# Kernel optimization log

Measured on AMD Instinct MI355X. Metric: run time of the kernel, lower is better.

Reference implementation:

```python
import jax, jax.numpy as jnp
import numpy as np

N, E, G = 50000, 800000, 1024      # nodes, edges, graphs
NF, R, H, O, B = 32, 4, 64, 16, 2  # node vocab, relations, hidden, output, conv blocks
MAX_DEG = 10                       # PyG MFConv default max_degree


def setup_inputs() -> dict:
    key = jax.random.key(0)
    ks = jax.random.split(key, 32)
    s = 0.05
    inp = {
        "x": jax.random.normal(ks[0], (N, NF), jnp.float32),
        "edge_attr": jax.random.normal(ks[1], (E, R), jnp.float32),
        "edge_index": jax.random.randint(ks[2], (2, E), 0, N),
        "batch_idx": jnp.sort(jax.random.randint(ks[3], (N,), 0, G)),
        "emb": jax.random.normal(ks[4], (NF, H), jnp.float32) * s,
        "lin1_w": jax.random.normal(ks[5], (H, H), jnp.float32) * s,
        "lin1_b": jnp.zeros((H,), jnp.float32),
        "lin2_w": jax.random.normal(ks[6], (H, O), jnp.float32) * s,
        "lin2_b": jnp.zeros((O,), jnp.float32),
    }
    for b in range(B):
        k = 7 + 4 * b
        inp[f"rgcn_w{b}"] = jax.random.normal(ks[k], (R, H, H), jnp.float32) * s
        inp[f"rgcn_root{b}"] = jax.random.normal(ks[k + 1], (H, H), jnp.float32) * s
        inp[f"rgcn_b{b}"] = jnp.zeros((H,), jnp.float32)
        inp[f"mf_wl{b}"] = jax.random.normal(ks[k + 2], (MAX_DEG + 1, H, H), jnp.float32) * s
        inp[f"mf_bl{b}"] = jnp.zeros((MAX_DEG + 1, H), jnp.float32)
        inp[f"mf_wr{b}"] = jax.random.normal(ks[k + 3], (MAX_DEG + 1, H, H), jnp.float32) * s
    return inp


def _rgcn(h, src, tgt, rel, W, Wroot, bias):
    # PyG RGCNConv: per-relation linear transform + per-(node,relation) MEAN aggregation + root + bias.
    hx = jnp.einsum('nh,rho->rno', h, W)            # [R,N,H] transformed features per relation
    m = hx[rel, src]                                # [E,H] per-edge messages
    seg = tgt * R + rel                             # segment id per (target node, relation)
    cnt = jax.ops.segment_sum(jnp.ones((E,), h.dtype), seg, num_segments=N * R)
    inv = jnp.where(cnt > 0, 1.0 / cnt, 0.0)
    agg = jax.ops.segment_sum(m * inv[seg][:, None], tgt, num_segments=N)
    return agg + h @ Wroot + bias


def _mfconv(h, src, tgt, Wl, bl, Wr):
    # PyG MFConv: sum-aggregate neighbors, then degree-indexed linear layers (lin_l has bias, lin_r none).
    deg = jnp.clip(jax.ops.segment_sum(jnp.ones((E,), jnp.int32), tgt, num_segments=N), 0, MAX_DEG)
    agg = jax.ops.segment_sum(h[src], tgt, num_segments=N)   # [N,H]
    out = jnp.zeros_like(h)
    for d in range(MAX_DEG + 1):                    # fixed small set of degree buckets
        mask = (deg == d)[:, None]
        out = out + jnp.where(mask, agg @ Wl[d] + bl[d] + h @ Wr[d], 0.0)
    return out


def reference(x, edge_index, edge_attr, batch_idx, emb,
              rgcn_w0, rgcn_root0, rgcn_b0, mf_wl0, mf_bl0, mf_wr0,
              rgcn_w1, rgcn_root1, rgcn_b1, mf_wl1, mf_bl1, mf_wr1,
              lin1_w, lin1_b, lin2_w, lin2_b):
    src, tgt = edge_index[0], edge_index[1]
    rel = jnp.argmax(edge_attr, axis=-1)
    h = emb[jnp.argmax(x, axis=-1)]                 # node embedding lookup
    blocks = [(rgcn_w0, rgcn_root0, rgcn_b0, mf_wl0, mf_bl0, mf_wr0),
              (rgcn_w1, rgcn_root1, rgcn_b1, mf_wl1, mf_bl1, mf_wr1)]
    for (W, Wro, bi, Wl, bl, Wr) in blocks:
        h = jax.nn.relu(h)
        h = _rgcn(h, src, tgt, rel, W, Wro, bi)
        h = jax.nn.relu(h)
        h = _mfconv(h, src, tgt, Wl, bl, Wr)
    g = jax.ops.segment_sum(h, batch_idx, num_segments=G)   # global add pool
    g = jax.nn.relu(g @ lin1_w + lin1_b)
    return g @ lin2_w + lin2_b
```

## Files before the change

kernel.cpp:

```cpp
#include <hip/hip_runtime.h>
#include <hip/hip_fp16.h>
#include <cstdint>
#include <cstddef>

#define Nn 50000
#define Ne 800000
#define Ng 1024
#define NFd 32
#define Rr 4
#define Hd 64
#define Od 16
#define MAXD 10
#define NSEG (Nn * Rr)
#define SCAN_BLK ((NSEG + 255) / 256)
#define ORDER_SZ (Nn + 48)
#define NB_MF ((ORDER_SZ + 15) / 16)
#define NB_RG (Nn / 16)
#define NB_RELSEG (Ne / 256)
#define NB_EMBED (Nn / 4)
#define WT_PER_LAYER (Hd * 5 * Hd)

typedef _Float16 f16x8 __attribute__((ext_vector_type(8)));
typedef float f32x4 __attribute__((ext_vector_type(4)));

__device__ __forceinline__ float reluf(float v) { return v > 0.f ? v : 0.f; }
__device__ __forceinline__ int rfl(int v) { return __builtin_amdgcn_readfirstlane(v); }

__global__ void k_rel_emb(const float4* __restrict__ ea, const int* __restrict__ eidx,
                          int* __restrict__ seg, int* __restrict__ rank,
                          int* __restrict__ cnt,
                          const float* __restrict__ x, const float* __restrict__ emb,
                          float* __restrict__ h, __half* __restrict__ h16) {
    if (blockIdx.x < NB_RELSEG) {
        int e = blockIdx.x * 256 + threadIdx.x;
        float4 a = ea[e];
        int bi = 0; float bv = a.x;
        if (a.y > bv) { bv = a.y; bi = 1; }
        if (a.z > bv) { bv = a.z; bi = 2; }
        if (a.w > bv) { bv = a.w; bi = 3; }
        int s = eidx[Ne + e] * Rr + bi;
        seg[e] = s;
        rank[e] = atomicAdd(&cnt[s], 1);
    } else {
        int wave = ((blockIdx.x - NB_RELSEG) * 256 + threadIdx.x) >> 6;
        int lane = threadIdx.x & 63;
        float v = (lane < NFd) ? x[(size_t)wave * NFd + lane] : -1e30f;
        int idx = lane;
        #pragma unroll
        for (int off = 16; off >= 1; off >>= 1) {
            float ov = __shfl_down(v, off);
            int oi = __shfl_down(idx, off);
            if (ov > v || (ov == v && oi < idx)) { v = ov; idx = oi; }
        }
        idx = __shfl(idx, 0);
        float hv = reluf(emb[(size_t)idx * Hd + lane]);
        h[(size_t)wave * Hd + lane] = hv;
        h16[(size_t)wave * Hd + lane] = __float2half(hv);
    }
}

__global__ void k_prep_wt(const float* __restrict__ w0, const float* __restrict__ r0,
                          const float* __restrict__ w1, const float* __restrict__ r1,
                          __half* __restrict__ wt) {
    int idx = blockIdx.x * 256 + threadIdx.x;
    if (idx >= 2 * WT_PER_LAYER) return;
    int b = idx / WT_PER_LAYER;
    int rem = idx % WT_PER_LAYER;
    int c = rem / 320;
    int k = rem % 320;
    const float* W  = b ? w1 : w0;
    const float* Rt = b ? r1 : r0;
    float v = (k < 64) ? Rt[k * Hd + c]
                       : W[((size_t)((k - 64) >> 6)) * Hd * Hd + ((k - 64) & 63) * Hd + c];
    wt[idx] = __float2half(v);
}

__global__ void k_scan1(const int* __restrict__ cnt, int* __restrict__ off,
                        int* __restrict__ bsum, int* __restrict__ bcnt) {
    __shared__ int s[256];
    __shared__ int hist[16];
    int t = threadIdx.x;
    if (t < 16) hist[t] = 0;
    int idx = blockIdx.x * 256 + t;
    int v = (idx < NSEG) ? cnt[idx] : 0;
    s[t] = v;
    __syncthreads();
    if ((t & 3) == 0 && idx < NSEG) {
        int dsum = s[t] + s[t + 1] + s[t + 2] + s[t + 3];
        atomicAdd(&hist[min(dsum, MAXD)], 1);
    }
    #pragma unroll
    for (int o = 1; o < 256; o <<= 1) {
        int x = (t >= o) ? s[t - o] : 0;
        __syncthreads();
        s[t] += x;
        __syncthreads();
    }
    if (idx < NSEG) off[idx] = s[t] - v;
    if (t == 255) bsum[blockIdx.x] = s[255];
    if (t < 16) {
        int h = hist[t];
        if (h > 0) atomicAdd(&bcnt[t], h);
    }
}

__global__ void k_scan2(int* __restrict__ bsum, const int* __restrict__ bcnt,
                        int* __restrict__ bbase, int* __restrict__ order) {
    __shared__ int s[1024];
    int t = threadIdx.x;
    int v = (t < SCAN_BLK) ? bsum[t] : 0;
    s[t] = v;
    __syncthreads();
    #pragma unroll
    for (int o = 1; o < 1024; o <<= 1) {
        int x = (t >= o) ? s[t - o] : 0;
        __syncthreads();
        s[t] += x;
        __syncthreads();
    }
    if (t < SCAN_BLK) bsum[t] = s[t] - v;
    if (t == 0) {
        int run = 0;
        for (int d = 0; d <= MAXD; d++) {
            int c = bcnt[d];
            bbase[d] = run;
            int pad = (c + 3) & ~3;
            for (int i = c; i < pad; i++) order[run + i] = -1;
            run += pad;
        }
        for (int i = run; i < ORDER_SZ; i++) order[i] = -1;
    }
}

__global__ void k_scan3_bucket(int* __restrict__ off, const int* __restrict__ bsum,
                               const int4* __restrict__ cnt4, const int* __restrict__ bbase,
                               int* __restrict__ bfill, int* __restrict__ order) {
    __shared__ int hist[16];
    __shared__ int base[16];
    int t = threadIdx.x;
    if (t < 16) hist[t] = 0;
    __syncthreads();
    int idx = blockIdx.x * 256 + t;
    if (idx == 0) off[NSEG] = Ne;
    if (idx < NSEG) off[idx] = off[idx] + bsum[blockIdx.x];
    int d = 0, rk = 0;
    bool valid = (idx < Nn);
    if (valid) {
        int4 c = cnt4[idx];
        d = min(c.x + c.y + c.z + c.w, MAXD);
        rk = atomicAdd(&hist[d], 1);
    }
    __syncthreads();
    if (t < 16) {
        int h = hist[t];
        base[t] = (h > 0) ? atomicAdd(&bfill[t], h) : 0;
    }
    __syncthreads();
    if (valid) order[bbase[d] + base[d] + rk] = idx | (d << 20);
}

__global__ void k_scatter(const int* __restrict__ eidx, const int* __restrict__ seg,
                          const int* __restrict__ rank, const int* __restrict__ off,
                          int* __restrict__ sorted_src) {
    int e = blockIdx.x * 256 + threadIdx.x;
    if (e >= Ne) return;
    int pos = off[seg[e]] + rank[e];
    sorted_src[pos] = eidx[e];
}

#define H16(ptr, s) __half2float((ptr)[(size_t)(s) * Hd + lane])

__global__ __launch_bounds__(256) void k_rgcn_fused(
        const __half* __restrict__ hin16,
        const int* __restrict__ off, const int* __restrict__ ssrc,
        const __half* __restrict__ wt, const float* __restrict__ bias,
        float* __restrict__ hout, __half* __restrict__ hout16) {
    __shared__ __align__(16) __half alds[16 * 296];
    int tid = threadIdx.x;
    int wv = tid >> 6, lane = tid & 63;
    int nblk = rfl(blockIdx.x * 16);
    int n0 = nblk + wv * 4;
    int ob[17];
    #pragma unroll
    for (int k = 0; k < 17; k++) ob[k] = rfl(off[4 * n0 + k]);

    float acc = 0.f, snap = 0.f;
    int segi = 0;
    int nb = ob[1];
    int e = ob[0], eEnd = ob[16];

#define EMIT_SEG do {                                                \
        float d_ = acc - snap; snap = acc;                           \
        int cN_ = ob[segi + 1] - ob[segi];                           \
        float iv_ = (cN_ > 0) ? 1.f / (float)cN_ : 0.f;              \
        alds[(wv * 4 + (segi >> 2)) * 296 + (segi & 3) * 72 + lane]  \
            = __float2half(d_ * iv_);                                \
        segi++;                                                      \
        nb = (segi < 16) ? ob[segi + 1] : 0x7fffffff;                \
    } while (0)

    if (e + 16 <= eEnd) {
        int4 iA = *(const int4*)(ssrc + e);
        int4 iB = *(const int4*)(ssrc + e + 4);
        int4 iC = *(const int4*)(ssrc + e + 8);
        int4 iD = *(const int4*)(ssrc + e + 12);
        while (true) {
            int en = e + 16;
            bool more = (en + 16 <= eEnd);
            int4 jA, jB, jC, jD;
            if (more) {
                jA = *(const int4*)(ssrc + en);
                jB = *(const int4*)(ssrc + en + 4);
                jC = *(const int4*)(ssrc + en + 8);
                jD = *(const int4*)(ssrc + en + 12);
            }
            float v0 = H16(hin16, iA.x);
            float v1 = H16(hin16, iA.y);
            float v2 = H16(hin16, iA.z);
            float v3 = H16(hin16, iA.w);
            float v4 = H16(hin16, iB.x);
            float v5 = H16(hin16, iB.y);
            float v6 = H16(hin16, iB.z);
            float v7 = H16(hin16, iB.w);
            float v8 = H16(hin16, iC.x);
            float v9 = H16(hin16, iC.y);
            float vA = H16(hin16, iC.z);
            float vB = H16(hin16, iC.w);
            float vC = H16(hin16, iD.x);
            float vD = H16(hin16, iD.y);
            float vE = H16(hin16, iD.z);
            float vF = H16(hin16, iD.w);
            while (e + 0  == nb) EMIT_SEG;  acc += v0;
            while (e + 1  == nb) EMIT_SEG;  acc += v1;
            while (e + 2  == nb) EMIT_SEG;  acc += v2;
            while (e + 3  == nb) EMIT_SEG;  acc += v3;
            while (e + 4  == nb) EMIT_SEG;  acc += v4;
            while (e + 5  == nb) EMIT_SEG;  acc += v5;
            while (e + 6  == nb) EMIT_SEG;  acc += v6;
            while (e + 7  == nb) EMIT_SEG;  acc += v7;
            while (e + 8  == nb) EMIT_SEG;  acc += v8;
            while (e + 9  == nb) EMIT_SEG;  acc += v9;
            while (e + 10 == nb) EMIT_SEG;  acc += vA;
            while (e + 11 == nb) EMIT_SEG;  acc += vB;
            while (e + 12 == nb) EMIT_SEG;  acc += vC;
            while (e + 13 == nb) EMIT_SEG;  acc += vD;
            while (e + 14 == nb) EMIT_SEG;  acc += vE;
            while (e + 15 == nb) EMIT_SEG;  acc += vF;
            e = en;
            if (!more) break;
            iA = jA; iB = jB; iC = jC; iD = jD;
        }
    }
    for (; e < eEnd; e++) {
        while (e == nb) EMIT_SEG;
        int s = rfl(ssrc[e]);
        acc += H16(hin16, s);
    }
    while (segi < 16) EMIT_SEG;
#undef EMIT_SEG

    __syncthreads();

    int rp = lane & 15;
    int g  = lane >> 4;
    const __half* ha = hin16 + (size_t)(nblk + rp) * Hd + 8 * g;
    const __half* ba = wt + (size_t)(wv * 16 + rp) * 320 + 8 * g;
    const __half* aa = alds + rp * 296 + 8 * g;
    f32x4 dacc = {0.f, 0.f, 0.f, 0.f};
    #pragma unroll
    for (int s = 0; s < 10; s++) {
        f16x8 bfrag = *(const f16x8*)(ba + s * 32);
        f16x8 afrag;
        if (s < 2) afrag = *(const f16x8*)(ha + s * 32);
        else       afrag = *(const f16x8*)(aa + ((s - 2) >> 1) * 72 + ((s - 2) & 1) * 32);
        dacc = __builtin_amdgcn_mfma_f32_16x16x32_f16(afrag, bfrag, dacc, 0, 0, 0);
    }
    int c = wv * 16 + rp;
    float bb = bias[c];
    #pragma unroll
    for (int j = 0; j < 4; j++) {
        int row = nblk + g * 4 + j;
        float v = reluf(dacc[j] + bb);
        hout[(size_t)row * Hd + c] = v;
        hout16[(size_t)row * Hd + c] = __float2half(v);
    }
}

__global__ __launch_bounds__(256) void k_mf_fused(
        const float* __restrict__ hin, const __half* __restrict__ hin16,
        const int* __restrict__ off, const int* __restrict__ ssrc,
        const int* __restrict__ order, const float* __restrict__ Wl,
        const float* __restrict__ bl, const float* __restrict__ Wr,
        float* __restrict__ hout, __half* __restrict__ hout16, int relu_out) {
    __shared__ float lds[4][4][Hd];
    int tid = threadIdx.x;
    int wv = tid >> 6, lane = tid & 63;
    int slot0 = rfl(blockIdx.x * 16 + wv * 4);
    int ent[4];
    #pragma unroll
    for (int i = 0; i < 4; i++) ent[i] = rfl(order[slot0 + i]);
    int d = -1;
    #pragma unroll
    for (int i = 3; i >= 0; i--) if (ent[i] >= 0) d = ent[i] >> 20;
    if (d < 0) return;
    int n[4];
    #pragma unroll
    for (int i = 0; i < 4; i++) n[i] = (ent[i] >= 0) ? (ent[i] & 0xFFFFF) : 0;
    for (int i = 0; i < 4; i++) {
        int e0 = rfl(off[n[i] * Rr]);
        int e4 = rfl(off[n[i] * Rr + Rr]);
        float p0 = 0.f, p1 = 0.f, p2 = 0.f, p3 = 0.f;
        int e = e0;
        for (; e + 16 <= e4; e += 16) {
            const int4 sA = *(const int4*)(ssrc + e);
            const int4 sB = *(const int4*)(ssrc + e + 4);
            const int4 sC = *(const int4*)(ssrc + e + 8);
            const int4 sD = *(const int4*)(ssrc + e + 12);
            p0 += H16(hin16, sA.x) + H16(hin16, sA.y) + H16(hin16, sA.z) + H16(hin16, sA.w);
            p1 += H16(hin16, sB.x) + H16(hin16, sB.y) + H16(hin16, sB.z) + H16(hin16, sB.w);
            p2 += H16(hin16, sC.x) + H16(hin16, sC.y) + H16(hin16, sC.z) + H16(hin16, sC.w);
            p3 += H16(hin16, sD.x) + H16(hin16, sD.y) + H16(hin16, sD.z) + H16(hin16, sD.w);
        }
        for (; e + 4 <= e4; e += 4) {
            const int4 sA = *(const int4*)(ssrc + e);
            p0 += H16(hin16, sA.x) + H16(hin16, sA.y) + H16(hin16, sA.z) + H16(hin16, sA.w);
        }
        for (; e < e4; e++) {
            int s = rfl(ssrc[e]);
            p0 += H16(hin16, s);
        }
        lds[wv][i][lane] = (p0 + p1) + (p2 + p3);
    }
    const float* wl = Wl + (size_t)d * Hd * Hd;
    const float* wr = Wr + (size_t)d * Hd * Hd;
    float acc[4] = {0.f, 0.f, 0.f, 0.f};
    for (int kc = 0; kc < Hd; kc += 4) {
        float a0 = wl[(kc + 0) * Hd + lane];
        float a1 = wl[(kc + 1) * Hd + lane];
        float a2 = wl[(kc + 2) * Hd + lane];
        float a3 = wl[(kc + 3) * Hd + lane];
        float b0 = wr[(kc + 0) * Hd + lane];
        float b1 = wr[(kc + 1) * Hd + lane];
        float b2 = wr[(kc + 2) * Hd + lane];
        float b3 = wr[(kc + 3) * Hd + lane];
        #pragma unroll
        for (int i = 0; i < 4; i++) {
            const float4 av = *(const float4*)(&lds[wv][i][kc]);
            const float4 hv = *(const float4*)(hin + (size_t)n[i] * Hd + kc);
            acc[i] += av.x * a0 + av.y * a1 + av.z * a2 + av.w * a3
                    + hv.x * b0 + hv.y * b1 + hv.z * b2 + hv.w * b3;
        }
    }
    float bb = bl[d * Hd + lane];
    #pragma unroll
    for (int i = 0; i < 4; i++)
        if (ent[i] >= 0) {
            float v = acc[i] + bb;
            if (relu_out) {
                v = reluf(v);
                hout16[(size_t)n[i] * Hd + lane] = __float2half(v);
            }
            hout[(size_t)n[i] * Hd + lane] = v;
        }
}

__global__ void k_pool(const float* __restrict__ h, const int* __restrict__ batch,
                       float* __restrict__ g) {
    int wave = rfl((blockIdx.x * 256 + threadIdx.x) >> 6);
    int lane = threadIdx.x & 63;
    int n0 = wave * 4;
    if (n0 >= Nn) return;
    int b0 = batch[n0], b1 = batch[n0 + 1], b2 = batch[n0 + 2], b3 = batch[n0 + 3];
    float v0 = h[(size_t)n0 * Hd + lane];
    float v1 = h[(size_t)(n0 + 1) * Hd + lane];
    float v2 = h[(size_t)(n0 + 2) * Hd + lane];
    float v3 = h[(size_t)(n0 + 3) * Hd + lane];
    if (b0 == b1 && b0 == b2 && b0 == b3) {
        unsafeAtomicAdd(&g[(size_t)b0 * Hd + lane], v0 + v1 + v2 + v3);
    } else {
        unsafeAtomicAdd(&g[(size_t)b0 * Hd + lane], v0);
        unsafeAtomicAdd(&g[(size_t)b1 * Hd + lane], v1);
        unsafeAtomicAdd(&g[(size_t)b2 * Hd + lane], v2);
        unsafeAtomicAdd(&g[(size_t)b3 * Hd + lane], v3);
    }
}

__global__ void k_head(const float* __restrict__ g, const float* __restrict__ w1,
                       const float* __restrict__ b1, const float* __restrict__ w2,
                       const float* __restrict__ b2, float* __restrict__ out) {
    __shared__ float t[4][Hd];
    int wv = threadIdx.x >> 6;
    int lane = threadIdx.x & 63;
    int gi = blockIdx.x * 4 + wv;
    float acc = b1[lane];
    for (int k = 0; k < Hd; k++) acc += g[(size_t)gi * Hd + k] * w1[k * Hd + lane];
    t[wv][lane] = reluf(acc);
    __syncthreads();
    if (lane < Od) {
        float o = b2[lane];
        for (int k = 0; k < Hd; k++) o += t[wv][k] * w2[k * Od + lane];
        out[(size_t)gi * Od + lane] = o;
    }
}

extern "C" void kernel_launch(void* const* d_in, const int* in_sizes, int n_in,
                              void* d_out, int out_size, void* d_ws, size_t ws_size,
                              hipStream_t stream) {
    const float* x      = (const float*)d_in[0];
    const float* ea     = (const float*)d_in[1];
    const int*   eidx   = (const int*)d_in[2];
    const int*   batch  = (const int*)d_in[3];
    const float* emb    = (const float*)d_in[4];
    const float* lin1_w = (const float*)d_in[5];
    const float* lin1_b = (const float*)d_in[6];
    const float* lin2_w = (const float*)d_in[7];
    const float* lin2_b = (const float*)d_in[8];
    const float* rgcn_w[2]    = {(const float*)d_in[9],  (const float*)d_in[15]};
    const float* rgcn_root[2] = {(const float*)d_in[10], (const float*)d_in[16]};
    const float* rgcn_b[2]    = {(const float*)d_in[11], (const float*)d_in[17]};
    const float* mf_wl[2]     = {(const float*)d_in[12], (const float*)d_in[18]};
    const float* mf_bl[2]     = {(const float*)d_in[13], (const float*)d_in[19]};
    const float* mf_wr[2]     = {(const float*)d_in[14], (const float*)d_in[20]};

    char* p = (char*)d_ws;
    float* h0    = (float*)p; p += sizeof(float) * (size_t)Nn * Hd;
    float* h1    = (float*)p; p += sizeof(float) * (size_t)Nn * Hd;
    __half* h16a = (__half*)p; p += sizeof(__half) * (size_t)Nn * Hd;
    __half* h16b = (__half*)p; p += sizeof(__half) * (size_t)Nn * Hd;
    float* gbuf  = (float*)p; p += sizeof(float) * (size_t)Ng * Hd;
    __half* wt16 = (__half*)p; p += sizeof(__half) * (size_t)2 * WT_PER_LAYER;
    int* seg     = (int*)p;   p += sizeof(int) * (size_t)Ne;
    int* rank    = (int*)p;   p += sizeof(int) * (size_t)Ne;
    int* ssrc    = (int*)p;   p += sizeof(int) * (size_t)Ne;
    int* cnt     = (int*)p;   p += sizeof(int) * (size_t)NSEG;
    int* bcnt    = (int*)p;   p += sizeof(int) * 16;
    int* bfill   = (int*)p;   p += sizeof(int) * 16;
    int* off     = (int*)p;   p += sizeof(int) * (size_t)(NSEG + 1);
    int* bsum    = (int*)p;   p += sizeof(int) * 1024;
    int* bbase   = (int*)p;   p += sizeof(int) * 16;
    int* order   = (int*)p;   p += sizeof(int) * (size_t)ORDER_SZ;

    hipMemsetAsync(cnt, 0, sizeof(int) * ((size_t)NSEG + 32), stream);
    hipMemsetAsync(gbuf, 0, sizeof(float) * (size_t)Ng * Hd, stream);

    k_prep_wt<<<(2 * WT_PER_LAYER + 255) / 256, 256, 0, stream>>>(
        rgcn_w[0], rgcn_root[0], rgcn_w[1], rgcn_root[1], wt16);
    k_rel_emb<<<NB_RELSEG + NB_EMBED, 256, 0, stream>>>((const float4*)ea, eidx, seg, rank,
                                                        cnt, x, emb, h0, h16a);
    k_scan1<<<SCAN_BLK, 256, 0, stream>>>(cnt, off, bsum, bcnt);
    k_scan2<<<1, 1024, 0, stream>>>(bsum, bcnt, bbase, order);
    k_scan3_bucket<<<SCAN_BLK, 256, 0, stream>>>(off, bsum, (const int4*)cnt, bbase,
                                                 bfill, order);
    k_scatter<<<Ne / 256, 256, 0, stream>>>(eidx, seg, rank, off, ssrc);

    float* hin = h0;   __half* hin16 = h16a;
    float* hout = h1;  __half* hout16 = h16b;
    for (int b = 0; b < 2; b++) {
        k_rgcn_fused<<<NB_RG, 256, 0, stream>>>(hin16, off, ssrc, wt16 + b * WT_PER_LAYER,
                                                rgcn_b[b], hout, hout16);
        k_mf_fused<<<NB_MF, 256, 0, stream>>>(hout, hout16, off, ssrc, order, mf_wl[b],
                                              mf_bl[b], mf_wr[b], hin, hin16,
                                              b == 0 ? 1 : 0);
    }
    k_pool<<<Nn / 16, 256, 0, stream>>>(hin, batch, gbuf);
    k_head<<<Ng / 4, 256, 0, stream>>>(gbuf, lin1_w, lin1_b, lin2_w, lin2_b, (float*)d_out);
}
```

Before: 363.0 us.

## Use fp16 MFMA for MFConv degree-bucketed linear layers with prepacked weights

The MFConv per-degree transform moves from a scalar fp32 FMA loop to 16x16x32 f16 MFMA instructions. Wl and Wr are prepacked into an fp16 [deg][col][128] layout in the prep kernel, and degree buckets are padded to 16 rows so each block handles a single degree. The kernel now reads the fp16 copy of h instead of fp32, and the embedding stage stops writing an fp32 h. This cuts FMA work and memory traffic at the cost of fp16 rounding on the aggregate and the root features, plus extra padding slots.

Result: no change. 356.0 us (-1.9%).

```diff
diff --git a/kernel.cpp b/kernel.cpp
--- a/kernel.cpp
+++ b/kernel.cpp
@@ -13,12 +13,14 @@
 #define MAXD 10
 #define NSEG (Nn * Rr)
 #define SCAN_BLK ((NSEG + 255) / 256)
-#define ORDER_SZ (Nn + 48)
-#define NB_MF ((ORDER_SZ + 15) / 16)
+#define ORDER_SZ (Nn + 176)
+#define NB_MF (ORDER_SZ / 16)
 #define NB_RG (Nn / 16)
 #define NB_RELSEG (Ne / 256)
 #define NB_EMBED (Nn / 4)
 #define WT_PER_LAYER (Hd * 5 * Hd)
+#define MFWT_PER_LAYER ((MAXD + 1) * Hd * 2 * Hd)
+#define PREP_TOTAL (2 * WT_PER_LAYER + 2 * MFWT_PER_LAYER)
 
 typedef _Float16 f16x8 __attribute__((ext_vector_type(8)));
 typedef float f32x4 __attribute__((ext_vector_type(4)));
@@ -30,7 +32,7 @@
                           int* __restrict__ seg, int* __restrict__ rank,
                           int* __restrict__ cnt,
                           const float* __restrict__ x, const float* __restrict__ emb,
-                          float* __restrict__ h, __half* __restrict__ h16) {
+                          __half* __restrict__ h16) {
     if (blockIdx.x < NB_RELSEG) {
         int e = blockIdx.x * 256 + threadIdx.x;
         float4 a = ea[e];
@@ -54,25 +56,40 @@
         }
         idx = __shfl(idx, 0);
         float hv = reluf(emb[(size_t)idx * Hd + lane]);
-        h[(size_t)wave * Hd + lane] = hv;
         h16[(size_t)wave * Hd + lane] = __float2half(hv);
     }
 }
 
-__global__ void k_prep_wt(const float* __restrict__ w0, const float* __restrict__ r0,
-                          const float* __restrict__ w1, const float* __restrict__ r1,
-                          __half* __restrict__ wt) {
+__global__ void k_prep(const float* __restrict__ w0, const float* __restrict__ r0,
+                       const float* __restrict__ w1, const float* __restrict__ r1,
+                       const float* __restrict__ wl0, const float* __restrict__ wr0,
+                       const float* __restrict__ wl1, const float* __restrict__ wr1,
+                       __half* __restrict__ wt, __half* __restrict__ mfwt) {
     int idx = blockIdx.x * 256 + threadIdx.x;
-    if (idx >= 2 * WT_PER_LAYER) return;
-    int b = idx / WT_PER_LAYER;
-    int rem = idx % WT_PER_LAYER;
-    int c = rem / 320;
-    int k = rem % 320;
-    const float* W  = b ? w1 : w0;
-    const float* Rt = b ? r1 : r0;
-    float v = (k < 64) ? Rt[k * Hd + c]
-                       : W[((size_t)((k - 64) >> 6)) * Hd * Hd + ((k - 64) & 63) * Hd + c];
-    wt[idx] = __float2half(v);
+    if (idx < 2 * WT_PER_LAYER) {
+        int b = idx / WT_PER_LAYER;
+        int rem = idx % WT_PER_LAYER;
+        int c = rem / 320;
+        int k = rem % 320;
+        const float* W  = b ? w1 : w0;
+        const float* Rt = b ? r1 : r0;
+        float v = (k < 64) ? Rt[k * Hd + c]
+                           : W[((size_t)((k - 64) >> 6)) * Hd * Hd + ((k - 64) & 63) * Hd + c];
+        wt[idx] = __float2half(v);
+    } else if (idx < PREP_TOTAL) {
+        int j = idx - 2 * WT_PER_LAYER;
+        int b = j / MFWT_PER_LAYER;
+        int rem = j % MFWT_PER_LAYER;
+        int d = rem / (Hd * 128);
+        int r2 = rem % (Hd * 128);
+        int c = r2 / 128;
+        int k = r2 % 128;
+        const float* Wl = b ? wl1 : wl0;
+        const float* Wr = b ? wr1 : wr0;
+        float v = (k < 64) ? Wl[(size_t)d * Hd * Hd + k * Hd + c]
+                           : Wr[(size_t)d * Hd * Hd + (k - 64) * Hd + c];
+        mfwt[j] = __float2half(v);
+    }
 }
 
 __global__ void k_scan1(const int* __restrict__ cnt, int* __restrict__ off,
@@ -124,7 +141,7 @@
         for (int d = 0; d <= MAXD; d++) {
             int c = bcnt[d];
             bbase[d] = run;
-            int pad = (c + 3) & ~3;
+            int pad = (c + 15) & ~15;
             for (int i = c; i < pad; i++) order[run + i] = -1;
             run += pad;
         }
@@ -287,81 +304,82 @@
 }
 
 __global__ __launch_bounds__(256) void k_mf_fused(
-        const float* __restrict__ hin, const __half* __restrict__ hin16,
+        const __half* __restrict__ hin16,
         const int* __restrict__ off, const int* __restrict__ ssrc,
-        const int* __restrict__ order, const float* __restrict__ Wl,
-        const float* __restrict__ bl, const float* __restrict__ Wr,
+        const int* __restrict__ order, const __half* __restrict__ mfwt,
+        const float* __restrict__ bl,
         float* __restrict__ hout, __half* __restrict__ hout16, int relu_out) {
-    __shared__ float lds[4][4][Hd];
+    __shared__ __align__(16) __half alds[16 * 72];
     int tid = threadIdx.x;
     int wv = tid >> 6, lane = tid & 63;
-    int slot0 = rfl(blockIdx.x * 16 + wv * 4);
-    int ent[4];
-    #pragma unroll
-    for (int i = 0; i < 4; i++) ent[i] = rfl(order[slot0 + i]);
-    int d = -1;
-    #pragma unroll
-    for (int i = 3; i >= 0; i--) if (ent[i] >= 0) d = ent[i] >> 20;
-    if (d < 0) return;
-    int n[4];
-    #pragma unroll
-    for (int i = 0; i < 4; i++) n[i] = (ent[i] >= 0) ? (ent[i] & 0xFFFFF) : 0;
+    int blk = rfl(blockIdx.x * 16);
+    int ent0 = rfl(order[blk]);
+    if (ent0 < 0) return;
+    int d = ent0 >> 20;
     for (int i = 0; i < 4; i++) {
-        int e0 = rfl(off[n[i] * Rr]);
-        int e4 = rfl(off[n[i] * Rr + Rr]);
-        float p0 = 0.f, p1 = 0.f, p2 = 0.f, p3 = 0.f;
-        int e = e0;
-        for (; e + 16 <= e4; e += 16) {
-            const int4 sA = *(const int4*)(ssrc + e);
-            const int4 sB = *(const int4*)(ssrc + e + 4);
-            const int4 sC = *(const int4*)(ssrc + e + 8);
-            const int4 sD = *(const int4*)(ssrc + e + 12);
-            p0 += H16(hin16, sA.x) + H16(hin16, sA.y) + H16(hin16, sA.z) + H16(hin16, sA.w);
-            p1 += H16(hin16, sB.x) + H16(hin16, sB.y) + H16(hin16, sB.z) + H16(hin16, sB.w);
-            p2 += H16(hin16, sC.x) + H16(hin16, sC.y) + H16(hin16, sC.z) + H16(hin16, sC.w);
-            p3 += H16(hin16, sD.x) + H16(hin16, sD.y) + H16(hin16, sD.z) + H16(hin16, sD.w);
+        int slot = blk + wv * 4 + i;
+        int ent = rfl(order[slot]);
+        float sum = 0.f;
+        if (ent >= 0) {
+            int n = ent & 0xFFFFF;
+            int e0 = rfl(off[n * Rr]);
+            int e4 = rfl(off[n * Rr + Rr]);
+            float p0 = 0.f, p1 = 0.f, p2 = 0.f, p3 = 0.f;
+            int e = e0;
+            for (; e + 16 <= e4; e += 16) {
+                const int4 sA = *(const int4*)(ssrc + e);
+                const int4 sB = *(const int4*)(ssrc + e + 4);
+                const int4 sC = *(const int4*)(ssrc + e + 8);
+                const int4 sD = *(const int4*)(ssrc + e + 12);
+                p0 += H16(hin16, sA.x) + H16(hin16, sA.y) + H16(hin16, sA.z) + H16(hin16, sA.w);
+                p1 += H16(hin16, sB.x) + H16(hin16, sB.y) + H16(hin16, sB.z) + H16(hin16, sB.w);
+                p2 += H16(hin16, sC.x) + H16(hin16, sC.y) + H16(hin16, sC.z) + H16(hin16, sC.w);
+                p3 += H16(hin16, sD.x) + H16(hin16, sD.y) + H16(hin16, sD.z) + H16(hin16, sD.w);
+            }
+            for (; e + 4 <= e4; e += 4) {
+                const int4 sA = *(const int4*)(ssrc + e);
+                p0 += H16(hin16, sA.x) + H16(hin16, sA.y) + H16(hin16, sA.z) + H16(hin16, sA.w);
+            }
+            for (; e < e4; e++) {
+                int s = rfl(ssrc[e]);
+                p0 += H16(hin16, s);
+            }
+            sum = (p0 + p1) + (p2 + p3);
         }
-        for (; e + 4 <= e4; e += 4) {
-            const int4 sA = *(const int4*)(ssrc + e);
-            p0 += H16(hin16, sA.x) + H16(hin16, sA.y) + H16(hin16, sA.z) + H16(hin16, sA.w);
-        }
-        for (; e < e4; e++) {
-            int s = rfl(ssrc[e]);
-            p0 += H16(hin16, s);
-        }
-        lds[wv][i][lane] = (p0 + p1) + (p2 + p3);
-    }
-    const float* wl = Wl + (size_t)d * Hd * Hd;
-    const float* wr = Wr + (size_t)d * Hd * Hd;
-    float acc[4] = {0.f, 0.f, 0.f, 0.f};
-    for (int kc = 0; kc < Hd; kc += 4) {
-        float a0 = wl[(kc + 0) * Hd + lane];
-        float a1 = wl[(kc + 1) * Hd + lane];
-        float a2 = wl[(kc + 2) * Hd + lane];
-        float a3 = wl[(kc + 3) * Hd + lane];
-        float b0 = wr[(kc + 0) * Hd + lane];
-        float b1 = wr[(kc + 1) * Hd + lane];
-        float b2 = wr[(kc + 2) * Hd + lane];
-        float b3 = wr[(kc + 3) * Hd + lane];
-        #pragma unroll
-        for (int i = 0; i < 4; i++) {
-            const float4 av = *(const float4*)(&lds[wv][i][kc]);
-            const float4 hv = *(const float4*)(hin + (size_t)n[i] * Hd + kc);
-            acc[i] += av.x * a0 + av.y * a1 + av.z * a2 + av.w * a3
-                    + hv.x * b0 + hv.y * b1 + hv.z * b2 + hv.w * b3;
-        }
-    }
-    float bb = bl[d * Hd + lane];
-    #pragma unroll
-    for (int i = 0; i < 4; i++)
-        if (ent[i] >= 0) {
-            float v = acc[i] + bb;
+        alds[(wv * 4 + i) * 72 + lane] = __float2half(sum);
+    }
+    __syncthreads();
+
+    int rp = lane & 15;
+    int g  = lane >> 4;
+    int entr = order[blk + rp];
+    int nr = (entr >= 0) ? (entr & 0xFFFFF) : 0;
+    const __half* aa = alds + rp * 72 + 8 * g;
+    const __half* ha = hin16 + (size_t)nr * Hd + 8 * g;
+    const __half* ba = mfwt + ((size_t)d * Hd + wv * 16 + rp) * 128 + 8 * g;
+    f32x4 dacc = {0.f, 0.f, 0.f, 0.f};
+    #pragma unroll
+    for (int s = 0; s < 4; s++) {
+        f16x8 bfrag = *(const f16x8*)(ba + s * 32);
+        f16x8 afrag = (s < 2) ? *(const f16x8*)(aa + s * 32)
+                              : *(const f16x8*)(ha + (s - 2) * 32);
+        dacc = __builtin_amdgcn_mfma_f32_16x16x32_f16(afrag, bfrag, dacc, 0, 0, 0);
+    }
+    int c = wv * 16 + rp;
+    float bb = bl[d * Hd + c];
+    #pragma unroll
+    for (int j = 0; j < 4; j++) {
+        int entw = order[blk + g * 4 + j];
+        if (entw >= 0) {
+            int n = entw & 0xFFFFF;
+            float v = dacc[j] + bb;
             if (relu_out) {
                 v = reluf(v);
-                hout16[(size_t)n[i] * Hd + lane] = __float2half(v);
+                hout16[(size_t)n * Hd + c] = __float2half(v);
             }
-            hout[(size_t)n[i] * Hd + lane] = v;
+            hout[(size_t)n * Hd + c] = v;
         }
+    }
 }
 
 __global__ void k_pool(const float* __restrict__ h, const int* __restrict__ batch,
@@ -429,6 +447,7 @@
     __half* h16b = (__half*)p; p += sizeof(__half) * (size_t)Nn * Hd;
     float* gbuf  = (float*)p; p += sizeof(float) * (size_t)Ng * Hd;
     __half* wt16 = (__half*)p; p += sizeof(__half) * (size_t)2 * WT_PER_LAYER;
+    __half* mfwt16 = (__half*)p; p += sizeof(__half) * (size_t)2 * MFWT_PER_LAYER;
     int* seg     = (int*)p;   p += sizeof(int) * (size_t)Ne;
     int* rank    = (int*)p;   p += sizeof(int) * (size_t)Ne;
     int* ssrc    = (int*)p;   p += sizeof(int) * (size_t)Ne;
@@ -443,25 +462,26 @@
     hipMemsetAsync(cnt, 0, sizeof(int) * ((size_t)NSEG + 32), stream);
     hipMemsetAsync(gbuf, 0, sizeof(float) * (size_t)Ng * Hd, stream);
 
-    k_prep_wt<<<(2 * WT_PER_LAYER + 255) / 256, 256, 0, stream>>>(
-        rgcn_w[0], rgcn_root[0], rgcn_w[1], rgcn_root[1], wt16);
+    k_prep<<<(PREP_TOTAL + 255) / 256, 256, 0, stream>>>(
+        rgcn_w[0], rgcn_root[0], rgcn_w[1], rgcn_root[1],
+        mf_wl[0], mf_wr[0], mf_wl[1], mf_wr[1], wt16, mfwt16);
     k_rel_emb<<<NB_RELSEG + NB_EMBED, 256, 0, stream>>>((const float4*)ea, eidx, seg, rank,
-                                                        cnt, x, emb, h0, h16a);
+                                                        cnt, x, emb, h16a);
     k_scan1<<<SCAN_BLK, 256, 0, stream>>>(cnt, off, bsum, bcnt);
     k_scan2<<<1, 1024, 0, stream>>>(bsum, bcnt, bbase, order);
     k_scan3_bucket<<<SCAN_BLK, 256, 0, stream>>>(off, bsum, (const int4*)cnt, bbase,
                                                  bfill, order);
     k_scatter<<<Ne / 256, 256, 0, stream>>>(eidx, seg, rank, off, ssrc);
 
-    float* hin = h0;   __half* hin16 = h16a;
-    float* hout = h1;  __half* hout16 = h16b;
+    float* h32a = h0;  float* h32b = h1;
+    __half* hin16 = h16a;  __half* hout16 = h16b;
     for (int b = 0; b < 2; b++) {
         k_rgcn_fused<<<NB_RG, 256, 0, stream>>>(hin16, off, ssrc, wt16 + b * WT_PER_LAYER,
-                                                rgcn_b[b], hout, hout16);
-        k_mf_fused<<<NB_MF, 256, 0, stream>>>(hout, hout16, off, ssrc, order, mf_wl[b],
-                                              mf_bl[b], mf_wr[b], hin, hin16,
-                                              b == 0 ? 1 : 0);
-    }
-    k_pool<<<Nn / 16, 256, 0, stream>>>(hin, batch, gbuf);
+                                                rgcn_b[b], h32b, hout16);
+        k_mf_fused<<<NB_MF, 256, 0, stream>>>(hout16, off, ssrc, order,
+                                              mfwt16 + b * MFWT_PER_LAYER, mf_bl[b],
+                                              h32a, hin16, b == 0 ? 1 : 0);
+    }
+    k_pool<<<Nn / 16, 256, 0, stream>>>(h32a, batch, gbuf);
     k_head<<<Ng / 4, 256, 0, stream>>>(gbuf, lin1_w, lin1_b, lin2_w, lin2_b, (float*)d_out);
 }
```
